# Kernel tuning notes

Hardware: AMD Instinct MI355X
Metric: run time of the kernel (lower is better)

## Reference

```python
import jax, jax.numpy as jnp
import numpy as np

N_TILE = 50000
N_POI = 50000
E = 200000
IN_F = 128
HID = 256
OUT = 256
HEADS = 8
NEG_SLOPE = 0.2


def gatv2(hs, hd, src, dst, Wsrc, bsrc, Wdst, bdst, attn, n_dst):
    """DGL GATv2Conv: per-edge LeakyReLU(fs_u + fd_v) attention, edge-softmax over
    incoming edges of each dst node, attention-weighted sum of source features.
    Returns (n_dst, H*D) (already flattened, matching .flatten(1))."""
    H, D = attn.shape
    fs = (hs @ Wsrc + bsrc).reshape(-1, H, D)  # (Ns, H, D)
    fd = (hd @ Wdst + bdst).reshape(-1, H, D)  # (Nd, H, D)
    e = jax.nn.leaky_relu(fs[src] + fd[dst], NEG_SLOPE)       # (E, H, D)
    logits = jnp.einsum('ehd,hd->eh', e, attn)                # (E, H)
    # segment softmax over destination neighborhoods
    mx = jax.ops.segment_max(logits, dst, num_segments=n_dst)  # (Nd, H)
    ex = jnp.exp(logits - mx[dst])
    den = jax.ops.segment_sum(ex, dst, num_segments=n_dst)
    alpha = ex / den[dst]                                      # (E, H)
    out = jax.ops.segment_sum(fs[src] * alpha[:, :, None], dst, num_segments=n_dst)
    return out.reshape(n_dst, H * D)


def hetero_layer(ht, hp, Wsrc, bsrc, Wdst, bdst, attn, idx, mean_agg):
    src_road, dst_road, src_tb, dst_tb, src_ct, dst_ct = idx
    m_road = gatv2(ht, ht, src_road, dst_road, Wsrc[0], bsrc[0], Wdst[0], bdst[0], attn[0], N_TILE)
    m_tb = gatv2(hp, ht, src_tb, dst_tb, Wsrc[1], bsrc[1], Wdst[1], bdst[1], attn[1], N_TILE)
    m_ct = gatv2(ht, hp, src_ct, dst_ct, Wsrc[2], bsrc[2], Wdst[2], bdst[2], attn[2], N_POI)
    tile = (m_road + m_tb) * (0.5 if mean_agg else 1.0)  # cross-relation sum/mean
    poi = m_ct  # single relation: sum == mean
    return jax.nn.relu(tile), jax.nn.relu(poi)


def _params(key, fan_in, fan_out, heads, dhead):
    ks = jax.random.split(key, 5)
    s = 1.0 / np.sqrt(fan_in)
    return (jax.random.normal(ks[0], (3, fan_in, fan_out), jnp.float32) * s,
            jnp.zeros((3, fan_out), jnp.float32),
            jax.random.normal(ks[1], (3, fan_in, fan_out), jnp.float32) * s,
            jnp.zeros((3, fan_out), jnp.float32),
            jax.random.normal(ks[2], (3, heads, dhead), jnp.float32) * s)


def setup_inputs() -> dict:
    key = jax.random.key(0)
    ks = jax.random.split(key, 12)
    inp = {
        'x_tile': jax.random.normal(ks[0], (N_TILE, IN_F), jnp.float32),
        'x_poi': jax.random.normal(ks[1], (N_POI, IN_F), jnp.float32),
        'src_road': jax.random.randint(ks[2], (E,), 0, N_TILE, jnp.int32),
        'dst_road': jax.random.randint(ks[3], (E,), 0, N_TILE, jnp.int32),
        'src_tb': jax.random.randint(ks[4], (E,), 0, N_POI, jnp.int32),
        'dst_tb': jax.random.randint(ks[5], (E,), 0, N_TILE, jnp.int32),
        'src_ct': jax.random.randint(ks[6], (E,), 0, N_TILE, jnp.int32),
        'dst_ct': jax.random.randint(ks[7], (E,), 0, N_POI, jnp.int32),
    }
    D = HID // HEADS
    for i, (fi, fo) in enumerate([(IN_F, HID), (HID, HID), (HID, OUT)]):
        Ws, bs, Wd, bd, at = _params(ks[8 + i], fi, fo, HEADS, fo // HEADS)
        inp[f'W_src_{i}'] = Ws; inp[f'b_src_{i}'] = bs
        inp[f'W_dst_{i}'] = Wd; inp[f'b_dst_{i}'] = bd
        inp[f'attn_{i}'] = at
    return inp


def reference(x_tile, x_poi, src_road, dst_road, src_tb, dst_tb, src_ct, dst_ct,
              W_src_0, b_src_0, W_dst_0, b_dst_0, attn_0,
              W_src_1, b_src_1, W_dst_1, b_dst_1, attn_1,
              W_src_2, b_src_2, W_dst_2, b_dst_2, attn_2):
    idx = (src_road, dst_road, src_tb, dst_tb, src_ct, dst_ct)
    ht, hp = hetero_layer(x_tile, x_poi, W_src_0, b_src_0, W_dst_0, b_dst_0, attn_0, idx, mean_agg=False)
    ht, hp = hetero_layer(ht, hp, W_src_1, b_src_1, W_dst_1, b_dst_1, attn_1, idx, mean_agg=True)
    ht, hp = hetero_layer(ht, hp, W_src_2, b_src_2, W_dst_2, b_dst_2, attn_2, idx, mean_agg=False)
    return ht, hp
```

## Files before the change

### kernel.cpp

```cpp
#include <hip/hip_runtime.h>
#include <hip/hip_bf16.h>

typedef __hip_bfloat16 bf16;

#define NT 50000
#define NP 50000
#define NE 200000
#define HH 8
#define DD 32
#define CC 256
#define NBLK 196

typedef short s8v __attribute__((ext_vector_type(8)));
typedef float f4v __attribute__((ext_vector_type(4)));

__device__ __forceinline__ float bu2f(unsigned short u) {
  return __uint_as_float(((unsigned)u) << 16);
}
__device__ __forceinline__ unsigned short f2bu(float x) {
  bf16 b = __float2bfloat16(x);
  return *(unsigned short*)&b;
}

__device__ __forceinline__ void gload_lds16(const void* g, void* l) {
  __builtin_amdgcn_global_load_lds(
      (const __attribute__((address_space(1))) void*)g,
      (__attribute__((address_space(3))) void*)l, 16, 0, 0);
}

__global__ __launch_bounds__(256) void cvt_f2b(const float* __restrict__ in,
                                               bf16* __restrict__ out, int n) {
  int i = blockIdx.x * 256 + threadIdx.x;
  if (i < n) out[i] = __float2bfloat16(in[i]);
}

struct WtArgs {
  const float* Ws[3]; const float* Wd[3];
  bf16* W1[3]; bf16* W2[3];
};
__global__ __launch_bounds__(256) void wt_cvt_all(WtArgs a) {
  int l = blockIdx.z, y = blockIdx.y;
  int K = (l == 0) ? 128 : 256;
  int idx = blockIdx.x * 256 + threadIdx.x;
  if (idx >= 256 * K) return;
  int n = idx / K, k = idx - n * K;
  const float* W; bf16* D; int dn;
  if (y == 0)      { W = a.Ws[l];                       D = a.W1[l]; dn = n; }
  else if (y == 1) { W = a.Wd[l];                       D = a.W1[l]; dn = n + 256; }
  else if (y == 2) { W = a.Wd[l] + (size_t)1 * K * 256; D = a.W1[l]; dn = n + 512; }
  else if (y == 3) { W = a.Ws[l] + (size_t)2 * K * 256; D = a.W1[l]; dn = n + 768; }
  else if (y == 4) { W = a.Ws[l] + (size_t)1 * K * 256; D = a.W2[l]; dn = n; }
  else             { W = a.Wd[l] + (size_t)2 * K * 256; D = a.W2[l]; dn = n + 256; }
  D[(size_t)dn * K + k] = __float2bfloat16(W[(size_t)k * 256 + n]);
}

struct BiArgs {
  const float* bs[3]; const float* bd[3];
  float* b1; float* b2;
};
__global__ __launch_bounds__(256) void bias_cat(BiArgs a) {
  int l = blockIdx.y, y = blockIdx.x;
  int n = threadIdx.x;
  float v;
  if (y == 0)      v = a.bs[l][n];
  else if (y == 1) v = a.bd[l][n];
  else if (y == 2) v = a.bd[l][256 + n];
  else if (y == 3) v = a.bs[l][512 + n];
  else if (y == 4) v = a.bs[l][256 + n];
  else             v = a.bd[l][512 + n];
  if (y < 4) a.b1[l * 1024 + y * 256 + n] = v;
  else       a.b2[l * 512 + (y - 4) * 256 + n] = v;
}

__global__ __launch_bounds__(256) void zero_i(int* __restrict__ p, int n) {
  int i = blockIdx.x * 256 + threadIdx.x;
  if (i < n) p[i] = 0;
}

__global__ __launch_bounds__(256) void hist3(
    const int* __restrict__ d0, const int* __restrict__ d1,
    const int* __restrict__ d2, int* __restrict__ deg) {
  int r = blockIdx.y;
  int e = blockIdx.x * 256 + threadIdx.x;
  if (e >= NE) return;
  const int* d = (r == 0) ? d0 : (r == 1) ? d1 : d2;
  atomicAdd(&deg[r * NT + d[e]], 1);
}

__global__ __launch_bounds__(256) void scan_s1(const int* __restrict__ deg,
                                               int* __restrict__ bsum) {
  __shared__ int buf[256];
  int r = blockIdx.y, b = blockIdx.x, t = threadIdx.x;
  int idx = b * 256 + t;
  buf[t] = (idx < NT) ? deg[r * NT + idx] : 0;
  __syncthreads();
  for (int s = 128; s > 0; s >>= 1) {
    if (t < s) buf[t] += buf[t + s];
    __syncthreads();
  }
  if (t == 0) bsum[r * NBLK + b] = buf[0];
}

__global__ __launch_bounds__(256) void scan_s2(
    const int* __restrict__ bsum, int* __restrict__ boff,
    int* __restrict__ offs) {
  __shared__ int buf[256];
  int t = threadIdx.x;
  for (int r = 0; r < 3; r++) {
    int v = (t < NBLK) ? bsum[r * NBLK + t] : 0;
    buf[t] = v;
    __syncthreads();
    for (int s = 1; s < 256; s <<= 1) {
      int u = (t >= s) ? buf[t - s] : 0;
      __syncthreads();
      buf[t] += u;
      __syncthreads();
    }
    if (t < NBLK) boff[r * NBLK + t] = buf[t] - v;
    if (t == 255) offs[(size_t)r * (NT + 1) + NT] = buf[255];
    __syncthreads();
  }
}

__global__ __launch_bounds__(256) void scan_s3(
    const int* __restrict__ deg, const int* __restrict__ boff,
    int* __restrict__ offs, int* __restrict__ cursor) {
  __shared__ int buf[256];
  int r = blockIdx.y, b = blockIdx.x, t = threadIdx.x;
  int idx = b * 256 + t;
  int v = (idx < NT) ? deg[r * NT + idx] : 0;
  buf[t] = v;
  __syncthreads();
  for (int s = 1; s < 256; s <<= 1) {
    int u = (t >= s) ? buf[t - s] : 0;
    __syncthreads();
    buf[t] += u;
    __syncthreads();
  }
  int o = boff[r * NBLK + b] + buf[t] - v;
  if (idx < NT) {
    offs[(size_t)r * (NT + 1) + idx] = o;
    cursor[r * NT + idx] = o;
  }
}

__global__ __launch_bounds__(256) void fill3(
    const int* __restrict__ d0, const int* __restrict__ d1,
    const int* __restrict__ d2, const int* __restrict__ s0,
    const int* __restrict__ s1, const int* __restrict__ s2,
    int* __restrict__ cursor, int* __restrict__ csrc) {
  int r = blockIdx.y;
  int e = blockIdx.x * 256 + threadIdx.x;
  if (e >= NE) return;
  const int* d = (r == 0) ? d0 : (r == 1) ? d1 : d2;
  const int* s = (r == 0) ? s0 : (r == 1) ? s1 : s2;
  int p = atomicAdd(&cursor[r * NT + d[e]], 1);
  csrc[(size_t)r * NE + p] = s[e];
}

__global__ __launch_bounds__(512, 2) void gemm256(
    const bf16* __restrict__ A1, const bf16* __restrict__ B1t,
    const float* __restrict__ bias1, bf16* __restrict__ C1,
    const bf16* __restrict__ A2, const bf16* __restrict__ B2t,
    const float* __restrict__ bias2, bf16* __restrict__ C2,
    int M, int K, int q8, int r8) {
  __shared__ short LDS[2][2][8192];
  int bid = blockIdx.x;
  int xcd = bid & 7, pos = bid >> 3;
  int wg = (xcd < r8 ? xcd * (q8 + 1) : r8 * (q8 + 1) + (xcd - r8) * q8) + pos;
  int bm = wg / 6, bn = wg - bm * 6;

  const bf16* A; const bf16* Bt; const float* bias; bf16* Cout; int Ncols, col0;
  if (bn < 4) { A = A1; Bt = B1t + (size_t)bn * 256 * K; bias = bias1; Cout = C1; Ncols = 1024; col0 = bn * 256; }
  else { A = A2; Bt = B2t + (size_t)(bn - 4) * 256 * K; bias = bias2; Cout = C2; Ncols = 512; col0 = (bn - 4) * 256; }

  int t = threadIdx.x;
  int lane = t & 63;
  int wid = t >> 6;
  int wm = wid >> 2, wn = wid & 3;
  int row0 = bm * 256;
  int wbase = t & ~63;

  f4v acc[4][8] = {};

  const bf16* Abase = A + (size_t)row0 * K;

  auto stage = [&](int buf, int kt) {
    int kofs = kt * 32;
    #pragma unroll
    for (int j = 0; j < 2; j++) {
      int s = j * 512 + t;
      int row = s >> 2, ch = s & 3;
      int sch = ch ^ ((row >> 1) & 3);
      gload_lds16(Abase + (size_t)row * K + kofs + sch * 8,
                  &LDS[buf][0][(j * 512 + wbase) * 8]);
    }
    #pragma unroll
    for (int j = 0; j < 2; j++) {
      int s = j * 512 + t;
      int row = s >> 2, ch = s & 3;
      int sch = ch ^ ((row >> 1) & 3);
      gload_lds16(Bt + (size_t)row * K + kofs + sch * 8,
                  &LDS[buf][1][(j * 512 + wbase) * 8]);
    }
  };

  int nk = K / 32;
  stage(0, 0);
  stage(1, 1);
  asm volatile("s_waitcnt vmcnt(4)" ::: "memory");
  __builtin_amdgcn_s_barrier();
  __builtin_amdgcn_sched_barrier(0);

  int cur = 0;
  for (int kt = 0; kt < nk; kt++) {
    int ch = lane >> 4;
    int rr = lane & 15;
    s8v af[4], bfv[8];
    #pragma unroll
    for (int i = 0; i < 4; i++) {
      int row = wn * 64 + i * 16 + rr;
      af[i] = *(const s8v*)&LDS[cur][1][(row * 4 + (ch ^ ((row >> 1) & 3))) * 8];
    }
    #pragma unroll
    for (int j = 0; j < 8; j++) {
      int row = wm * 128 + j * 16 + rr;
      bfv[j] = *(const s8v*)&LDS[cur][0][(row * 4 + (ch ^ ((row >> 1) & 3))) * 8];
    }
    asm volatile("s_waitcnt lgkmcnt(0)" ::: "memory");
    __builtin_amdgcn_s_barrier();
    __builtin_amdgcn_sched_barrier(0);
    bool staged = (kt + 2 < nk);
    if (staged) stage(cur, kt + 2);
    #pragma unroll
    for (int i = 0; i < 4; i++)
      #pragma unroll
      for (int j = 0; j < 8; j++)
        acc[i][j] = __builtin_amdgcn_mfma_f32_16x16x32_bf16(
            af[i], bfv[j], acc[i][j], 0, 0, 0);
    if (kt + 1 < nk) {
      if (staged) {
        asm volatile("s_waitcnt vmcnt(4)" ::: "memory");
      } else {
        asm volatile("s_waitcnt vmcnt(0)" ::: "memory");
      }
      __builtin_amdgcn_s_barrier();
      __builtin_amdgcn_sched_barrier(0);
    }
    cur ^= 1;
  }

  short* CL = &LDS[0][0][0];
  unsigned short* Cu = (unsigned short*)Cout;
  int q = lane >> 4, rr = lane & 15;
  #pragma unroll
  for (int p = 0; p < 2; p++) {
    __syncthreads();
    if (wm == p) {
      #pragma unroll
      for (int j = 0; j < 8; j++) {
        int row = j * 16 + rr;
        #pragma unroll
        for (int i = 0; i < 4; i++) {
          int n0 = wn * 64 + i * 16 + q * 4;
          float4 bv = *(const float4*)(bias + col0 + n0);
          ushort4 v = make_ushort4(f2bu(acc[i][j][0] + bv.x),
                                   f2bu(acc[i][j][1] + bv.y),
                                   f2bu(acc[i][j][2] + bv.z),
                                   f2bu(acc[i][j][3] + bv.w));
          int g = n0 >> 2;
          int slot = (g >> 1) ^ (row & 15);
          *(ushort4*)(CL + row * 256 + slot * 8 + (g & 1) * 4) = v;
        }
      }
    }
    __syncthreads();
    {
      int row = t >> 2, seg = t & 3;
      int grow = row0 + p * 128 + row;
      if (grow < M) {
        #pragma unroll
        for (int j2 = 0; j2 < 8; j2++) {
          int slot = j2 * 4 + seg;
          int slot_s = slot ^ (row & 15);
          s8v v = *(const s8v*)(CL + row * 256 + slot_s * 8);
          *(s8v*)&Cu[(size_t)grow * Ncols + col0 + slot * 8] = v;
        }
      }
    }
  }
}

__device__ __forceinline__ float edge_logit(
    ushort4 u, float d0, float d1, float d2, float d3, float4 at,
    float& f0, float& f1, float& f2, float& f3) {
  f0 = bu2f(u.x); f1 = bu2f(u.y); f2 = bu2f(u.z); f3 = bu2f(u.w);
  float t0 = f0 + d0; t0 = t0 > 0.f ? t0 : 0.2f * t0;
  float t1 = f1 + d1; t1 = t1 > 0.f ? t1 : 0.2f * t1;
  float t2 = f2 + d2; t2 = t2 > 0.f ? t2 : 0.2f * t2;
  float t3 = f3 + d3; t3 = t3 > 0.f ? t3 : 0.2f * t3;
  float lg = t0 * at.x + t1 * at.y + t2 * at.z + t3 * at.w;
  lg += __shfl_xor(lg, 1);
  lg += __shfl_xor(lg, 2);
  lg += __shfl_xor(lg, 4);
  return lg;
}

__device__ __forceinline__ float4 gat_pass(
    int e0, int e1, const int* __restrict__ csrc,
    const unsigned short* __restrict__ base, size_t stride,
    float d0, float d1, float d2, float d3, float4 at) {
  float m = -1e30f, den = 0.f;
  float a0 = 0.f, a1 = 0.f, a2 = 0.f, a3 = 0.f;
  int e = e0;
  for (; e + 4 <= e1; e += 4) {
    int s0 = csrc[e], s1 = csrc[e + 1], s2 = csrc[e + 2], s3 = csrc[e + 3];
    ushort4 u0 = *(const ushort4*)(base + (size_t)s0 * stride);
    ushort4 u1 = *(const ushort4*)(base + (size_t)s1 * stride);
    ushort4 u2 = *(const ushort4*)(base + (size_t)s2 * stride);
    ushort4 u3 = *(const ushort4*)(base + (size_t)s3 * stride);
    float f0, f1, f2, f3, g0, g1, g2, g3, h0, h1, h2, h3, i0, i1, i2, i3;
    float lg0 = edge_logit(u0, d0, d1, d2, d3, at, f0, f1, f2, f3);
    float lg1 = edge_logit(u1, d0, d1, d2, d3, at, g0, g1, g2, g3);
    float lg2 = edge_logit(u2, d0, d1, d2, d3, at, h0, h1, h2, h3);
    float lg3 = edge_logit(u3, d0, d1, d2, d3, at, i0, i1, i2, i3);
    float mn = fmaxf(fmaxf(fmaxf(lg0, lg1), fmaxf(lg2, lg3)), m);
    float c = __expf(m - mn);
    float x0 = __expf(lg0 - mn);
    float x1 = __expf(lg1 - mn);
    float x2 = __expf(lg2 - mn);
    float x3 = __expf(lg3 - mn);
    den = den * c + x0 + x1 + x2 + x3;
    a0 = a0 * c + x0 * f0 + x1 * g0 + x2 * h0 + x3 * i0;
    a1 = a1 * c + x0 * f1 + x1 * g1 + x2 * h1 + x3 * i1;
    a2 = a2 * c + x0 * f2 + x1 * g2 + x2 * h2 + x3 * i2;
    a3 = a3 * c + x0 * f3 + x1 * g3 + x2 * h3 + x3 * i3;
    m = mn;
  }
  for (; e < e1; ++e) {
    int s0 = csrc[e];
    ushort4 u0 = *(const ushort4*)(base + (size_t)s0 * stride);
    float f0, f1, f2, f3;
    float lg0 = edge_logit(u0, d0, d1, d2, d3, at, f0, f1, f2, f3);
    float mn = fmaxf(m, lg0);
    float c = __expf(m - mn);
    float x0 = __expf(lg0 - mn);
    den = den * c + x0;
    a0 = a0 * c + x0 * f0;
    a1 = a1 * c + x0 * f1;
    a2 = a2 * c + x0 * f2;
    a3 = a3 * c + x0 * f3;
    m = mn;
  }
  float inv = (den > 0.f) ? 1.f / den : 0.f;
  return make_float4(a0 * inv, a1 * inv, a2 * inv, a3 * inv);
}

__global__ __launch_bounds__(256) void node_gat_all(
    const int* __restrict__ offs, const int* __restrict__ csrc,
    const bf16* __restrict__ F1, const bf16* __restrict__ F2,
    const float* __restrict__ attnL, float scale,
    bf16* __restrict__ ht_n, bf16* __restrict__ hp_n,
    float* __restrict__ outT, float* __restrict__ outP) {
  int gw = blockIdx.x * 4 + (threadIdx.x >> 6);
  int lane = threadIdx.x & 63;
  int off = (lane >> 3) * DD + (lane & 7) * 4;
  const unsigned short* F1u = (const unsigned short*)F1;
  const unsigned short* F2u = (const unsigned short*)F2;

  if (gw < NT) {
    ushort4 udA = *(const ushort4*)(F1u + (size_t)gw * 1024 + 256 + off);
    float4 atA = *(const float4*)(attnL + off);
    float4 ra = gat_pass(offs[gw], offs[gw + 1], csrc, F1u + off, 1024,
                         bu2f(udA.x), bu2f(udA.y), bu2f(udA.z), bu2f(udA.w), atA);

    const int* offsB = offs + (NT + 1);
    ushort4 udB = *(const ushort4*)(F1u + (size_t)gw * 1024 + 512 + off);
    float4 atB = *(const float4*)(attnL + 256 + off);
    float4 rb = gat_pass(offsB[gw], offsB[gw + 1], csrc + NE, F2u + off, 512,
                         bu2f(udB.x), bu2f(udB.y), bu2f(udB.z), bu2f(udB.w), atB);

    float v0 = (ra.x + rb.x) * scale; v0 = v0 > 0.f ? v0 : 0.f;
    float v1 = (ra.y + rb.y) * scale; v1 = v1 > 0.f ? v1 : 0.f;
    float v2 = (ra.z + rb.z) * scale; v2 = v2 > 0.f ? v2 : 0.f;
    float v3 = (ra.w + rb.w) * scale; v3 = v3 > 0.f ? v3 : 0.f;

    size_t base = (size_t)gw * CC + off;
    if (ht_n)
      *(ushort4*)((unsigned short*)ht_n + base) =
          make_ushort4(f2bu(v0), f2bu(v1), f2bu(v2), f2bu(v3));
    if (outT) *(float4*)(outT + base) = make_float4(v0, v1, v2, v3);
  } else {
    int w = gw - NT;
    const int* offsC = offs + 2 * (NT + 1);
    ushort4 ud = *(const ushort4*)(F2u + (size_t)w * 512 + 256 + off);
    float4 at = *(const float4*)(attnL + 512 + off);
    float4 r = gat_pass(offsC[w], offsC[w + 1], csrc + 2 * (size_t)NE,
                        F1u + 768 + off, 1024,
                        bu2f(ud.x), bu2f(ud.y), bu2f(ud.z), bu2f(ud.w), at);

    float v0 = r.x > 0.f ? r.x : 0.f;
    float v1 = r.y > 0.f ? r.y : 0.f;
    float v2 = r.z > 0.f ? r.z : 0.f;
    float v3 = r.w > 0.f ? r.w : 0.f;

    size_t base = (size_t)w * CC + off;
    if (hp_n)
      *(ushort4*)((unsigned short*)hp_n + base) =
          make_ushort4(f2bu(v0), f2bu(v1), f2bu(v2), f2bu(v3));
    if (outP) *(float4*)(outP + base) = make_float4(v0, v1, v2, v3);
  }
}

extern "C" void kernel_launch(void* const* d_in, const int* in_sizes, int n_in,
                              void* d_out, int out_size, void* d_ws, size_t ws_size,
                              hipStream_t stream) {
  const float* x_tile = (const float*)d_in[0];
  const float* x_poi  = (const float*)d_in[1];
  const int* src_road = (const int*)d_in[2];
  const int* dst_road = (const int*)d_in[3];
  const int* src_tb   = (const int*)d_in[4];
  const int* dst_tb   = (const int*)d_in[5];
  const int* src_ct   = (const int*)d_in[6];
  const int* dst_ct   = (const int*)d_in[7];
  const float* Wsrc[3] = {(const float*)d_in[8],  (const float*)d_in[13], (const float*)d_in[18]};
  const float* bsrc[3] = {(const float*)d_in[9],  (const float*)d_in[14], (const float*)d_in[19]};
  const float* Wdst[3] = {(const float*)d_in[10], (const float*)d_in[15], (const float*)d_in[20]};
  const float* bdst[3] = {(const float*)d_in[11], (const float*)d_in[16], (const float*)d_in[21]};
  const float* attn[3] = {(const float*)d_in[12], (const float*)d_in[17], (const float*)d_in[22]};

  bf16* hbuf = (bf16*)d_ws;
  bf16* ht2[2] = {hbuf, hbuf + (size_t)NT * CC};
  bf16* hp2[2] = {hbuf + 2 * (size_t)NT * CC, hbuf + 3 * (size_t)NT * CC};
  bf16* F1 = hbuf + 4 * (size_t)NT * CC;
  bf16* F2 = F1 + (size_t)NT * 1024;
  int* offs = (int*)(F2 + (size_t)NT * 512);
  int* deg  = offs + 3 * (NT + 1);
  int* csrc = deg + 3 * NT;
  int* bsum = csrc + (size_t)3 * NE;
  int* boff = bsum + 3 * NBLK;
  uintptr_t wp = ((uintptr_t)(boff + 3 * NBLK) + 63) & ~(uintptr_t)63;
  bf16* W1c[3], *W2c[3];
  {
    bf16* w = (bf16*)wp;
    for (int l = 0; l < 3; l++) {
      int K = (l == 0) ? 128 : 256;
      W1c[l] = w; w += (size_t)1024 * K;
      W2c[l] = w; w += (size_t)512 * K;
    }
    wp = (uintptr_t)w;
  }
  float* b1 = (float*)((wp + 63) & ~(uintptr_t)63);
  float* b2 = b1 + 3 * 1024;

  cvt_f2b<<<(NT * 128 + 255) / 256, 256, 0, stream>>>(x_tile, ht2[0], NT * 128);
  cvt_f2b<<<(NP * 128 + 255) / 256, 256, 0, stream>>>(x_poi, hp2[0], NP * 128);

  {
    WtArgs wa;
    BiArgs ba;
    for (int l = 0; l < 3; l++) {
      wa.Ws[l] = Wsrc[l]; wa.Wd[l] = Wdst[l];
      wa.W1[l] = W1c[l];  wa.W2[l] = W2c[l];
      ba.bs[l] = bsrc[l]; ba.bd[l] = bdst[l];
    }
    ba.b1 = b1; ba.b2 = b2;
    dim3 gw(256, 6, 3);
    wt_cvt_all<<<gw, 256, 0, stream>>>(wa);
    dim3 gb(6, 3);
    bias_cat<<<gb, 256, 0, stream>>>(ba);
  }

  zero_i<<<(3 * NT + 255) / 256, 256, 0, stream>>>(deg, 3 * NT);
  {
    dim3 ge((NE + 255) / 256, 3);
    hist3<<<ge, 256, 0, stream>>>(dst_road, dst_tb, dst_ct, deg);
    dim3 gn(NBLK, 3);
    scan_s1<<<gn, 256, 0, stream>>>(deg, bsum);
    scan_s2<<<1, 256, 0, stream>>>(bsum, boff, offs);
    scan_s3<<<gn, 256, 0, stream>>>(deg, boff, offs, deg);
    fill3<<<ge, 256, 0, stream>>>(dst_road, dst_tb, dst_ct,
                                  src_road, src_tb, src_ct, deg, csrc);
  }

  int cb = 0;
  for (int l = 0; l < 3; l++) {
    int K = (l == 0) ? 128 : 256;
    bf16* ht_c = ht2[cb], *hp_c = hp2[cb];
    bf16* ht_n = (l == 2) ? nullptr : ht2[cb ^ 1];
    bf16* hp_n = (l == 2) ? nullptr : hp2[cb ^ 1];
    float st = (l == 1) ? 0.5f : 1.0f;
    float* outT = (l == 2) ? (float*)d_out : nullptr;
    float* outP = (l == 2) ? ((float*)d_out + (size_t)NT * CC) : nullptr;

    int NW = NBLK * 6, q8 = NW / 8, r8 = NW % 8;
    gemm256<<<NW, 512, 0, stream>>>(
        ht_c, W1c[l], b1 + l * 1024, F1,
        hp_c, W2c[l], b2 + l * 512,  F2,
        NT, K, q8, r8);

    node_gat_all<<<(NT + NP) / 4, 256, 0, stream>>>(
        offs, csrc, F1, F2, attn[l], st, ht_n, hp_n, outT, outP);

    cb ^= 1;
  }
}
```

Baseline: 591.4 us.

## Split node GAT aggregation across two waves per node and prescale source byte offsets

The GAT aggregation kernel now runs two wavefronts per destination node. Tile nodes put one relation on each wave, and POI nodes split their edge range in half. The partial online-softmax states are combined through shared memory after a block barrier. Source indices are stored pre-shifted into byte offsets, the exp is replaced by exp2 with log2e folded into the attention vector, and the scalar remainder loop is replaced by clamped 4-wide iterations. This doubles the number of waves to expose more memory parallelism, at the cost of LDS traffic, a barrier, and idle second waves during the final combine.

```diff
diff --git a/kernel.cpp b/kernel.cpp
--- a/kernel.cpp
+++ b/kernel.cpp
@@ -10,6 +10,7 @@
 #define DD 32
 #define CC 256
 #define NBLK 196
+#define LOG2E 1.4426950408889634f
 
 typedef short s8v __attribute__((ext_vector_type(8)));
 typedef float f4v __attribute__((ext_vector_type(4)));
@@ -148,14 +149,15 @@
     const int* __restrict__ d0, const int* __restrict__ d1,
     const int* __restrict__ d2, const int* __restrict__ s0,
     const int* __restrict__ s1, const int* __restrict__ s2,
-    int* __restrict__ cursor, int* __restrict__ csrc) {
+    int* __restrict__ cursor, int* __restrict__ csrcb) {
   int r = blockIdx.y;
   int e = blockIdx.x * 256 + threadIdx.x;
   if (e >= NE) return;
   const int* d = (r == 0) ? d0 : (r == 1) ? d1 : d2;
   const int* s = (r == 0) ? s0 : (r == 1) ? s1 : s2;
+  int shift = (r == 1) ? 10 : 11;
   int p = atomicAdd(&cursor[r * NT + d[e]], 1);
-  csrc[(size_t)r * NE + p] = s[e];
+  csrcb[(size_t)r * NE + p] = s[e] << shift;
 }
 
 __global__ __launch_bounds__(512, 2) void gemm256(
@@ -306,30 +308,31 @@
   return lg;
 }
 
-__device__ __forceinline__ float4 gat_pass(
-    int e0, int e1, const int* __restrict__ csrc,
-    const unsigned short* __restrict__ base, size_t stride,
-    float d0, float d1, float d2, float d3, float4 at) {
-  float m = -1e30f, den = 0.f;
-  float a0 = 0.f, a1 = 0.f, a2 = 0.f, a3 = 0.f;
-  int e = e0;
-  for (; e + 4 <= e1; e += 4) {
-    int s0 = csrc[e], s1 = csrc[e + 1], s2 = csrc[e + 2], s3 = csrc[e + 3];
-    ushort4 u0 = *(const ushort4*)(base + (size_t)s0 * stride);
-    ushort4 u1 = *(const ushort4*)(base + (size_t)s1 * stride);
-    ushort4 u2 = *(const ushort4*)(base + (size_t)s2 * stride);
-    ushort4 u3 = *(const ushort4*)(base + (size_t)s3 * stride);
+__device__ __forceinline__ void gat_partial(
+    int s0, int s1, const int* __restrict__ csrcb,
+    const char* __restrict__ base,
+    float d0, float d1, float d2, float d3, float4 at,
+    float& m, float& den, float& a0, float& a1, float& a2, float& a3) {
+  m = -1e30f; den = 0.f;
+  a0 = 0.f; a1 = 0.f; a2 = 0.f; a3 = 0.f;
+  int last = s1 - 1;
+  for (int e = s0; e < s1; e += 4) {
+    int e1i = min(e + 1, last), e2i = min(e + 2, last), e3i = min(e + 3, last);
+    ushort4 u0 = *(const ushort4*)(base + csrcb[e]);
+    ushort4 u1 = *(const ushort4*)(base + csrcb[e1i]);
+    ushort4 u2 = *(const ushort4*)(base + csrcb[e2i]);
+    ushort4 u3 = *(const ushort4*)(base + csrcb[e3i]);
     float f0, f1, f2, f3, g0, g1, g2, g3, h0, h1, h2, h3, i0, i1, i2, i3;
     float lg0 = edge_logit(u0, d0, d1, d2, d3, at, f0, f1, f2, f3);
     float lg1 = edge_logit(u1, d0, d1, d2, d3, at, g0, g1, g2, g3);
     float lg2 = edge_logit(u2, d0, d1, d2, d3, at, h0, h1, h2, h3);
     float lg3 = edge_logit(u3, d0, d1, d2, d3, at, i0, i1, i2, i3);
     float mn = fmaxf(fmaxf(fmaxf(lg0, lg1), fmaxf(lg2, lg3)), m);
-    float c = __expf(m - mn);
-    float x0 = __expf(lg0 - mn);
-    float x1 = __expf(lg1 - mn);
-    float x2 = __expf(lg2 - mn);
-    float x3 = __expf(lg3 - mn);
+    float c = exp2f(m - mn);
+    float x0 = exp2f(lg0 - mn);
+    float x1 = (e + 1 <= last) ? exp2f(lg1 - mn) : 0.f;
+    float x2 = (e + 2 <= last) ? exp2f(lg2 - mn) : 0.f;
+    float x3 = (e + 3 <= last) ? exp2f(lg3 - mn) : 0.f;
     den = den * c + x0 + x1 + x2 + x3;
     a0 = a0 * c + x0 * f0 + x1 * g0 + x2 * h0 + x3 * i0;
     a1 = a1 * c + x0 * f1 + x1 * g1 + x2 * h1 + x3 * i1;
@@ -337,78 +340,100 @@
     a3 = a3 * c + x0 * f3 + x1 * g3 + x2 * h3 + x3 * i3;
     m = mn;
   }
-  for (; e < e1; ++e) {
-    int s0 = csrc[e];
-    ushort4 u0 = *(const ushort4*)(base + (size_t)s0 * stride);
-    float f0, f1, f2, f3;
-    float lg0 = edge_logit(u0, d0, d1, d2, d3, at, f0, f1, f2, f3);
-    float mn = fmaxf(m, lg0);
-    float c = __expf(m - mn);
-    float x0 = __expf(lg0 - mn);
-    den = den * c + x0;
-    a0 = a0 * c + x0 * f0;
-    a1 = a1 * c + x0 * f1;
-    a2 = a2 * c + x0 * f2;
-    a3 = a3 * c + x0 * f3;
-    m = mn;
-  }
-  float inv = (den > 0.f) ? 1.f / den : 0.f;
-  return make_float4(a0 * inv, a1 * inv, a2 * inv, a3 * inv);
 }
 
 __global__ __launch_bounds__(256) void node_gat_all(
-    const int* __restrict__ offs, const int* __restrict__ csrc,
+    const int* __restrict__ offs, const int* __restrict__ csrcb,
     const bf16* __restrict__ F1, const bf16* __restrict__ F2,
     const float* __restrict__ attnL, float scale,
     bf16* __restrict__ ht_n, bf16* __restrict__ hp_n,
     float* __restrict__ outT, float* __restrict__ outP) {
+  __shared__ float rbuf[2][64][6];
   int gw = blockIdx.x * 4 + (threadIdx.x >> 6);
   int lane = threadIdx.x & 63;
   int off = (lane >> 3) * DD + (lane & 7) * 4;
+  int pair = threadIdx.x >> 7;
   const unsigned short* F1u = (const unsigned short*)F1;
   const unsigned short* F2u = (const unsigned short*)F2;
 
-  if (gw < NT) {
-    ushort4 udA = *(const ushort4*)(F1u + (size_t)gw * 1024 + 256 + off);
-    float4 atA = *(const float4*)(attnL + off);
-    float4 ra = gat_pass(offs[gw], offs[gw + 1], csrc, F1u + off, 1024,
-                         bu2f(udA.x), bu2f(udA.y), bu2f(udA.z), bu2f(udA.w), atA);
-
-    const int* offsB = offs + (NT + 1);
-    ushort4 udB = *(const ushort4*)(F1u + (size_t)gw * 1024 + 512 + off);
-    float4 atB = *(const float4*)(attnL + 256 + off);
-    float4 rb = gat_pass(offsB[gw], offsB[gw + 1], csrc + NE, F2u + off, 512,
-                         bu2f(udB.x), bu2f(udB.y), bu2f(udB.z), bu2f(udB.w), atB);
-
-    float v0 = (ra.x + rb.x) * scale; v0 = v0 > 0.f ? v0 : 0.f;
-    float v1 = (ra.y + rb.y) * scale; v1 = v1 > 0.f ? v1 : 0.f;
-    float v2 = (ra.z + rb.z) * scale; v2 = v2 > 0.f ? v2 : 0.f;
-    float v3 = (ra.w + rb.w) * scale; v3 = v3 > 0.f ? v3 : 0.f;
-
-    size_t base = (size_t)gw * CC + off;
-    if (ht_n)
-      *(ushort4*)((unsigned short*)ht_n + base) =
-          make_ushort4(f2bu(v0), f2bu(v1), f2bu(v2), f2bu(v3));
-    if (outT) *(float4*)(outT + base) = make_float4(v0, v1, v2, v3);
+  bool isTile = (gw < 2 * NT);
+  int node, sub;
+  if (isTile) { node = gw >> 1; sub = gw & 1; }
+  else { int w = gw - 2 * NT; node = w >> 1; sub = w & 1; }
+
+  const int* po; const int* pcb; const char* pb; int udofs; int atofs;
+  if (isTile) {
+    po = sub ? (offs + (NT + 1)) : offs;
+    pcb = sub ? (csrcb + NE) : csrcb;
+    pb = sub ? ((const char*)F2u + off * 2) : ((const char*)F1u + off * 2);
+    udofs = sub ? 512 : 256;
+    atofs = sub ? 256 : 0;
   } else {
-    int w = gw - NT;
-    const int* offsC = offs + 2 * (NT + 1);
-    ushort4 ud = *(const ushort4*)(F2u + (size_t)w * 512 + 256 + off);
-    float4 at = *(const float4*)(attnL + 512 + off);
-    float4 r = gat_pass(offsC[w], offsC[w + 1], csrc + 2 * (size_t)NE,
-                        F1u + 768 + off, 1024,
-                        bu2f(ud.x), bu2f(ud.y), bu2f(ud.z), bu2f(ud.w), at);
-
-    float v0 = r.x > 0.f ? r.x : 0.f;
-    float v1 = r.y > 0.f ? r.y : 0.f;
-    float v2 = r.z > 0.f ? r.z : 0.f;
-    float v3 = r.w > 0.f ? r.w : 0.f;
-
-    size_t base = (size_t)w * CC + off;
-    if (hp_n)
-      *(ushort4*)((unsigned short*)hp_n + base) =
-          make_ushort4(f2bu(v0), f2bu(v1), f2bu(v2), f2bu(v3));
-    if (outP) *(float4*)(outP + base) = make_float4(v0, v1, v2, v3);
+    po = offs + 2 * (NT + 1);
+    pcb = csrcb + 2 * (size_t)NE;
+    pb = (const char*)F1u + (768 + off) * 2;
+    udofs = -1;
+    atofs = 512;
+  }
+
+  ushort4 ud;
+  if (isTile)
+    ud = *(const ushort4*)(F1u + (size_t)node * 1024 + udofs + off);
+  else
+    ud = *(const ushort4*)(F2u + (size_t)node * 512 + 256 + off);
+  float4 at = *(const float4*)(attnL + atofs + off);
+  at.x *= LOG2E; at.y *= LOG2E; at.z *= LOG2E; at.w *= LOG2E;
+
+  int s0 = po[node], s1 = po[node + 1];
+  if (!isTile) {
+    int mid = s0 + ((s1 - s0 + 1) >> 1);
+    if (sub) s0 = mid; else s1 = mid;
+  }
+
+  float m, den, a0, a1, a2, a3;
+  gat_partial(s0, s1, pcb, pb, bu2f(ud.x), bu2f(ud.y), bu2f(ud.z), bu2f(ud.w),
+              at, m, den, a0, a1, a2, a3);
+
+  if (sub) {
+    rbuf[pair][lane][0] = m;  rbuf[pair][lane][1] = den;
+    rbuf[pair][lane][2] = a0; rbuf[pair][lane][3] = a1;
+    rbuf[pair][lane][4] = a2; rbuf[pair][lane][5] = a3;
+  }
+  __syncthreads();
+  if (!sub) {
+    float v0, v1, v2, v3;
+    if (isTile) {
+      float inv1 = (den > 0.f) ? 1.f / den : 0.f;
+      float d2v = rbuf[pair][lane][1];
+      float inv2 = (d2v > 0.f) ? 1.f / d2v : 0.f;
+      v0 = (a0 * inv1 + rbuf[pair][lane][2] * inv2) * scale;
+      v1 = (a1 * inv1 + rbuf[pair][lane][3] * inv2) * scale;
+      v2 = (a2 * inv1 + rbuf[pair][lane][4] * inv2) * scale;
+      v3 = (a3 * inv1 + rbuf[pair][lane][5] * inv2) * scale;
+    } else {
+      float m2 = rbuf[pair][lane][0], den2 = rbuf[pair][lane][1];
+      float M = fmaxf(m, m2);
+      float c1 = exp2f(m - M), c2 = exp2f(m2 - M);
+      float D = den * c1 + den2 * c2;
+      float inv = (D > 0.f) ? 1.f / D : 0.f;
+      v0 = (a0 * c1 + rbuf[pair][lane][2] * c2) * inv;
+      v1 = (a1 * c1 + rbuf[pair][lane][3] * c2) * inv;
+      v2 = (a2 * c1 + rbuf[pair][lane][4] * c2) * inv;
+      v3 = (a3 * c1 + rbuf[pair][lane][5] * c2) * inv;
+    }
+    v0 = v0 > 0.f ? v0 : 0.f;
+    v1 = v1 > 0.f ? v1 : 0.f;
+    v2 = v2 > 0.f ? v2 : 0.f;
+    v3 = v3 > 0.f ? v3 : 0.f;
+    size_t base = (size_t)node * CC + off;
+    ushort4 o = make_ushort4(f2bu(v0), f2bu(v1), f2bu(v2), f2bu(v3));
+    if (isTile) {
+      if (ht_n) *(ushort4*)((unsigned short*)ht_n + base) = o;
+      if (outT) *(float4*)(outT + base) = make_float4(v0, v1, v2, v3);
+    } else {
+      if (hp_n) *(ushort4*)((unsigned short*)hp_n + base) = o;
+      if (outP) *(float4*)(outP + base) = make_float4(v0, v1, v2, v3);
+    }
   }
 }
 
@@ -436,8 +461,8 @@
   bf16* F2 = F1 + (size_t)NT * 1024;
   int* offs = (int*)(F2 + (size_t)NT * 512);
   int* deg  = offs + 3 * (NT + 1);
-  int* csrc = deg + 3 * NT;
-  int* bsum = csrc + (size_t)3 * NE;
+  int* csrcb = deg + 3 * NT;
+  int* bsum = csrcb + (size_t)3 * NE;
   int* boff = bsum + 3 * NBLK;
   uintptr_t wp = ((uintptr_t)(boff + 3 * NBLK) + 63) & ~(uintptr_t)63;
   bf16* W1c[3], *W2c[3];
@@ -480,7 +505,7 @@
     scan_s2<<<1, 256, 0, stream>>>(bsum, boff, offs);
     scan_s3<<<gn, 256, 0, stream>>>(deg, boff, offs, deg);
     fill3<<<ge, 256, 0, stream>>>(dst_road, dst_tb, dst_ct,
-                                  src_road, src_tb, src_ct, deg, csrc);
+                                  src_road, src_tb, src_ct, deg, csrcb);
   }
 
   int cb = 0;
@@ -499,8 +524,8 @@
         hp_c, W2c[l], b2 + l * 512,  F2,
         NT, K, q8, r8);
 
-    node_gat_all<<<(NT + NP) / 4, 256, 0, stream>>>(
-        offs, csrc, F1, F2, attn[l], st, ht_n, hp_n, outT, outP);
+    node_gat_all<<<(2 * NT + 2 * NP) / 4, 256, 0, stream>>>(
+        offs, csrcb, F1, F2, attn[l], st, ht_n, hp_n, outT, outP);
 
     cb ^= 1;
   }
```

New measurement: 617.2 us. 1.04x slower.
